# Performance work log

Hardware: AMD Instinct MI355X
Metric: run time of the kernel (lower is better)

The kernel has to match this reference:

```python
import jax, jax.numpy as jnp
import numpy as np

N_HEAD = 16
D_MODEL = 1024
HEAD_DIM = D_MODEL // N_HEAD
B, S = 2, 2048


def setup_inputs() -> dict:
    key = jax.random.key(0)
    ks = jax.random.split(key, 7)
    qry = jax.random.normal(ks[0], (B, S, D_MODEL), dtype=jnp.float32)
    k_in = jax.random.normal(ks[1], (B, S, D_MODEL), dtype=jnp.float32)
    v_in = jax.random.normal(ks[2], (B, S, D_MODEL), dtype=jnp.float32)
    # causal boolean mask (B, S_q, S_k) as asserted in SelfAttention.forward
    attn_mask = jnp.broadcast_to(jnp.tril(jnp.ones((S, S), dtype=bool)), (B, S, S))
    scale = 1.0 / np.sqrt(D_MODEL)
    Wq = jax.random.normal(ks[3], (D_MODEL, D_MODEL), dtype=jnp.float32) * scale
    Wk = jax.random.normal(ks[4], (D_MODEL, D_MODEL), dtype=jnp.float32) * scale
    Wv = jax.random.normal(ks[5], (D_MODEL, D_MODEL), dtype=jnp.float32) * scale
    Wo = jax.random.normal(ks[6], (D_MODEL, D_MODEL), dtype=jnp.float32) * scale
    return {"qry": qry, "key": k_in, "val": v_in, "attn_mask": attn_mask,
            "Wq": Wq, "Wk": Wk, "Wv": Wv, "Wo": Wo}


def reference(qry, key, val, attn_mask, Wq, Wk, Wv, Wo):
    Bq, Sq, _ = qry.shape
    # torch Linear: y = x @ W.T (no bias)
    q = (qry @ Wq.T).reshape(Bq, Sq, N_HEAD, HEAD_DIM).transpose(0, 2, 1, 3)
    k = (key @ Wk.T).reshape(Bq, -1, N_HEAD, HEAD_DIM).transpose(0, 2, 1, 3)
    v = (val @ Wv.T).reshape(Bq, -1, N_HEAD, HEAD_DIM).transpose(0, 2, 1, 3)
    # scores: [B, H, Sq, Sk]
    scores = jnp.einsum('bhqd,bhkd->bhqk', q, k) / jnp.sqrt(jnp.float32(HEAD_DIM * N_HEAD) / N_HEAD)
    # attn_bias: 0 where mask True, -inf where False; broadcast over heads
    bias = jnp.where(attn_mask[:, None, :, :], 0.0, -jnp.inf).astype(scores.dtype)
    attn_weights = jax.nn.softmax(scores + bias, axis=-1)
    attn_feats = jnp.einsum('bhqk,bhkd->bhqd', attn_weights, v)
    attn_feats = attn_feats.transpose(0, 2, 1, 3).reshape(Bq, Sq, D_MODEL)
    output = attn_feats @ Wo.T
    return output, attn_weights
```

## Files before the change

kernel.cpp:

```cpp
#include <hip/hip_runtime.h>
#include <hip/hip_bf16.h>
#include <cstdint>
#include <cstddef>

#define DM 1024
#define NH 16
#define HD 64
#define BB 2
#define SS 2048

typedef __attribute__((ext_vector_type(4))) float f32x4;
typedef __attribute__((ext_vector_type(8))) short bf16x8;

typedef __attribute__((address_space(1))) const void GV;
typedef __attribute__((address_space(3))) void LV;

#define WAITV(N) asm volatile("s_waitcnt vmcnt(" N ")" ::: "memory")
#define SBAR do { __builtin_amdgcn_s_barrier(); asm volatile("" ::: "memory"); } while (0)

__global__ __launch_bounds__(256) void cvt_all(
    const float* s0, const float* s1, const float* s2, const float* s3,
    const float* s4, const float* s5, const float* s6,
    __hip_bfloat16* d0, __hip_bfloat16* d1, __hip_bfloat16* d2, __hip_bfloat16* d3,
    __hip_bfloat16* d4, __hip_bfloat16* d5, __hip_bfloat16* d6) {
    const float* s; __hip_bfloat16* d; int n4;
    switch (blockIdx.y) {
        case 0: s = s0; d = d0; n4 = 1 << 20; break;
        case 1: s = s1; d = d1; n4 = 1 << 20; break;
        case 2: s = s2; d = d2; n4 = 1 << 20; break;
        case 3: s = s3; d = d3; n4 = 1 << 18; break;
        case 4: s = s4; d = d4; n4 = 1 << 18; break;
        case 5: s = s5; d = d5; n4 = 1 << 18; break;
        default: s = s6; d = d6; n4 = 1 << 18; break;
    }
    for (int i = blockIdx.x * 256 + threadIdx.x; i < n4; i += 1024 * 256) {
        float4 v = reinterpret_cast<const float4*>(s)[i];
        ushort4 o;
        o.x = __builtin_bit_cast(unsigned short, __float2bfloat16(v.x));
        o.y = __builtin_bit_cast(unsigned short, __float2bfloat16(v.y));
        o.z = __builtin_bit_cast(unsigned short, __float2bfloat16(v.z));
        o.w = __builtin_bit_cast(unsigned short, __float2bfloat16(v.w));
        reinterpret_cast<ushort4*>(d)[i] = o;
    }
}

template <typename OutT>
__device__ __forceinline__ void gemm_body(const __hip_bfloat16* __restrict__ A,
                                          const __hip_bfloat16* __restrict__ Bw,
                                          OutT* __restrict__ C, int M, int N, int K,
                                          float alpha,
                                          __hip_bfloat16* As, __hip_bfloat16* Bs) {
    const int lane = threadIdx.x & 63;
    const int wv = threadIdx.x >> 6;
    const int wr = wv >> 1, wc = wv & 1;
    const int g = lane >> 4, cq = lane & 15;
    const int tM = blockIdx.y * 128, tN = blockIdx.x * 128;

    f32x4 acc[4][4];
#pragma unroll
    for (int i = 0; i < 4; ++i)
#pragma unroll
        for (int j = 0; j < 4; ++j) acc[i][j] = (f32x4){0.f, 0.f, 0.f, 0.f};

    for (int k0 = 0; k0 < K; k0 += 32) {
        __syncthreads();
#pragma unroll
        for (int r = 0; r < 2; ++r) {
            int chunk = r * 256 + wv * 64 + lane;
            int row = chunk >> 2;
            int kk = (chunk & 3) * 8;
            __builtin_amdgcn_global_load_lds((GV*)(A + (size_t)(tM + row) * K + k0 + kk),
                                             (LV*)(As + (size_t)(r * 256 + wv * 64) * 8), 16, 0, 0);
            __builtin_amdgcn_global_load_lds((GV*)(Bw + (size_t)(tN + row) * K + k0 + kk),
                                             (LV*)(Bs + (size_t)(r * 256 + wv * 64) * 8), 16, 0, 0);
        }
        __syncthreads();

        bf16x8 af[4], bfr[4];
#pragma unroll
        for (int i = 0; i < 4; ++i)
            af[i] = *reinterpret_cast<const bf16x8*>(As + (wr * 64 + i * 16 + cq) * 32 + g * 8);
#pragma unroll
        for (int j = 0; j < 4; ++j)
            bfr[j] = *reinterpret_cast<const bf16x8*>(Bs + (wc * 64 + j * 16 + cq) * 32 + g * 8);
#pragma unroll
        for (int i = 0; i < 4; ++i)
#pragma unroll
            for (int j = 0; j < 4; ++j)
                acc[i][j] = __builtin_amdgcn_mfma_f32_16x16x32_bf16(af[i], bfr[j], acc[i][j], 0, 0, 0);
    }

#pragma unroll
    for (int i = 0; i < 4; ++i)
#pragma unroll
        for (int j = 0; j < 4; ++j)
#pragma unroll
            for (int rr = 0; rr < 4; ++rr) {
                int row = tM + wr * 64 + i * 16 + g * 4 + rr;
                int col = tN + wc * 64 + j * 16 + cq;
                float v = acc[i][j][rr] * alpha;
                if constexpr (__is_same(OutT, float)) {
                    C[(size_t)row * N + col] = v;
                } else {
                    C[(size_t)row * N + col] = __float2bfloat16(v);
                }
            }
}

#define QALPHA 0.1803368801111204f

__global__ __launch_bounds__(256) void gemm_qkv(
    const __hip_bfloat16* qa, const __hip_bfloat16* ka, const __hip_bfloat16* va,
    const __hip_bfloat16* wq, const __hip_bfloat16* wk, const __hip_bfloat16* wv,
    __hip_bfloat16* Qm, __hip_bfloat16* Km, __hip_bfloat16* Vm) {
    __shared__ __hip_bfloat16 As[128 * 32];
    __shared__ __hip_bfloat16 Bs[128 * 32];
    const __hip_bfloat16 *A, *Bw;
    __hip_bfloat16* C;
    float alpha = 1.0f;
    switch (blockIdx.z) {
        case 0: A = qa; Bw = wq; C = Qm; alpha = QALPHA; break;
        case 1: A = ka; Bw = wk; C = Km; break;
        default: A = va; Bw = wv; C = Vm; break;
    }
    gemm_body<__hip_bfloat16>(A, Bw, C, BB * SS, DM, DM, alpha, As, Bs);
}

__global__ __launch_bounds__(256) void gemm_out(const __hip_bfloat16* __restrict__ A,
                                                const __hip_bfloat16* __restrict__ Bw,
                                                float* __restrict__ C) {
    __shared__ __hip_bfloat16 As[128 * 32];
    __shared__ __hip_bfloat16 Bs[128 * 32];
    gemm_body<float>(A, Bw, C, BB * SS, DM, DM, 1.0f, As, Bs);
}

__global__ __launch_bounds__(256) void transpose_v(const __hip_bfloat16* __restrict__ V,
                                                   __hip_bfloat16* __restrict__ VT) {
    const int bh = blockIdx.x;
    const int b = bh >> 4, h = bh & 15;
    const int k0 = blockIdx.y * 64;
    __shared__ __hip_bfloat16 tile[64][68];
    const int r = threadIdx.x >> 4;
    const int c4 = threadIdx.x & 15;
#pragma unroll
    for (int rr = r; rr < 64; rr += 16) {
        ushort4 u = *reinterpret_cast<const ushort4*>(
            V + (size_t)(b * SS + k0 + rr) * DM + h * HD + c4 * 4);
        *reinterpret_cast<ushort4*>(&tile[rr][c4 * 4]) = u;
    }
    __syncthreads();
#pragma unroll
    for (int dd = r; dd < 64; dd += 16) {
        ushort4 o;
        o.x = __builtin_bit_cast(unsigned short, tile[c4 * 4 + 0][dd]);
        o.y = __builtin_bit_cast(unsigned short, tile[c4 * 4 + 1][dd]);
        o.z = __builtin_bit_cast(unsigned short, tile[c4 * 4 + 2][dd]);
        o.w = __builtin_bit_cast(unsigned short, tile[c4 * 4 + 3][dd]);
        *reinterpret_cast<ushort4*>(VT + ((size_t)bh * HD + dd) * SS + k0 + c4 * 4) = o;
    }
}

__global__ __launch_bounds__(256) void attn_fused(const __hip_bfloat16* __restrict__ Q,
                                                  const __hip_bfloat16* __restrict__ Kb,
                                                  const __hip_bfloat16* __restrict__ VT,
                                                  float* __restrict__ Wout,
                                                  __hip_bfloat16* __restrict__ feats) {
    __shared__ __hip_bfloat16 sbuf[4][64 * 64];
    __shared__ __hip_bfloat16 plds[4][16][64];
    const int qt = (SS / 64 - 1) - blockIdx.x;
    const int bh = blockIdx.y;
    const int b = bh >> 4, h = bh & 15;
    const int lane = threadIdx.x & 63;
    const int wv = threadIdx.x >> 6;
    const int g = lane >> 4, cq = lane & 15;
    const int q0w = qt * 64 + wv * 16;
    const size_t rowbase = (size_t)b * SS;
    const int tmaxw = q0w >> 4;

    const __hip_bfloat16* qp = Q + (rowbase + q0w + cq) * DM + h * HD + g * 8;
    const bf16x8 qf0 = *reinterpret_cast<const bf16x8*>(qp);
    const bf16x8 qf1 = *reinterpret_cast<const bf16x8*>(qp + 32);

    auto stageK = [&](int kc, __hip_bfloat16* dst) {
#pragma unroll
        for (int i = 0; i < 2; ++i) {
            int slot = i * 256 + wv * 64 + lane;
            int row = slot >> 3, c16 = slot & 7;
            const __hip_bfloat16* src =
                Kb + (rowbase + kc * 64 + row) * DM + h * HD + ((c16 ^ (row & 7)) << 3);
            __builtin_amdgcn_global_load_lds(
                (GV*)src, (LV*)(dst + (size_t)(i * 256 + wv * 64) * 8), 16, 0, 0);
        }
    };
    auto stageV = [&](int kc, __hip_bfloat16* dst) {
#pragma unroll
        for (int i = 0; i < 2; ++i) {
            int slot = i * 256 + wv * 64 + lane;
            int row = slot >> 3, c16 = slot & 7;
            const __hip_bfloat16* src =
                VT + ((size_t)bh * HD + row) * SS + kc * 64 + ((c16 ^ (row & 7)) << 3);
            __builtin_amdgcn_global_load_lds(
                (GV*)src, (LV*)(dst + (size_t)(i * 256 + wv * 64) * 8), 16, 0, 0);
        }
    };

    const int swx = cq & 7;

    float l_[4] = {0.f, 0.f, 0.f, 0.f};
    stageK(0, sbuf[0]);
    stageK(qt < 1 ? qt : 1, sbuf[1]);
    stageK(qt < 2 ? qt : 2, sbuf[2]);
    WAITV("4");
    SBAR;
    for (int kc = 0; kc <= qt; ++kc) {
        const int nx = kc + 3;
        stageK(nx > qt ? qt : nx, sbuf[nx & 3]);
        const __hip_bfloat16* kbase = sbuf[kc & 3];
#pragma unroll
        for (int hh = 0; hh < 4; ++hh) {
            const int kt = kc * 4 + hh;
            if (kt > tmaxw) break;
            const __hip_bfloat16* kb = kbase + (hh * 16 + cq) * 64;
            bf16x8 kf0 = *reinterpret_cast<const bf16x8*>(kb + ((g ^ swx) << 3));
            bf16x8 kf1 = *reinterpret_cast<const bf16x8*>(kb + (((4 + g) ^ swx) << 3));
            f32x4 sc = (f32x4){0.f, 0.f, 0.f, 0.f};
            sc = __builtin_amdgcn_mfma_f32_16x16x32_bf16(qf0, kf0, sc, 0, 0, 0);
            sc = __builtin_amdgcn_mfma_f32_16x16x32_bf16(qf1, kf1, sc, 0, 0, 0);
            const int kk = kt * 16 + cq;
#pragma unroll
            for (int r = 0; r < 4; ++r) {
                const int qr = q0w + g * 4 + r;
                l_[r] += (kk <= qr) ? __builtin_amdgcn_exp2f(sc[r]) : 0.0f;
            }
        }
        if (kc < qt) {
            WAITV("4");
            SBAR;
        }
    }
    float invl[4];
#pragma unroll
    for (int r = 0; r < 4; ++r) {
        float l = l_[r];
#pragma unroll
        for (int mk = 1; mk < 16; mk <<= 1) l += __shfl_xor(l, mk);
        invl[r] = __builtin_amdgcn_rcpf(l);
    }

    f32x4 oacc[4];
#pragma unroll
    for (int j = 0; j < 4; ++j) oacc[j] = (f32x4){0.f, 0.f, 0.f, 0.f};

    SBAR;
    stageK(0, sbuf[0]);
    stageV(0, sbuf[2]);
    WAITV("0");
    SBAR;
    for (int kc = 0; kc <= qt; ++kc) {
        const int nx = kc + 1;
        const int nc = nx > qt ? qt : nx;
        stageK(nc, sbuf[nx & 1]);
        stageV(nc, sbuf[2 + (nx & 1)]);
        const __hip_bfloat16* kbase = sbuf[kc & 1];
        const __hip_bfloat16* vbase = sbuf[2 + (kc & 1)];

#pragma unroll
        for (int hh = 0; hh < 4; ++hh) {
            const int kt = kc * 4 + hh;
            if (kt <= tmaxw) {
                const __hip_bfloat16* kb = kbase + (hh * 16 + cq) * 64;
                bf16x8 kf0 = *reinterpret_cast<const bf16x8*>(kb + ((g ^ swx) << 3));
                bf16x8 kf1 = *reinterpret_cast<const bf16x8*>(kb + (((4 + g) ^ swx) << 3));
                f32x4 sc = (f32x4){0.f, 0.f, 0.f, 0.f};
                sc = __builtin_amdgcn_mfma_f32_16x16x32_bf16(qf0, kf0, sc, 0, 0, 0);
                sc = __builtin_amdgcn_mfma_f32_16x16x32_bf16(qf1, kf1, sc, 0, 0, 0);
                const int kk = kt * 16 + cq;
#pragma unroll
                for (int r = 0; r < 4; ++r) {
                    const int row = g * 4 + r;
                    const int qr = q0w + row;
                    float w = (kk <= qr) ? __builtin_amdgcn_exp2f(sc[r]) * invl[r] : 0.0f;
                    plds[wv][row][(hh * 16 + cq) ^ (8 * (row & 7))] = __float2bfloat16(w);
                }
            } else {
#pragma unroll
                for (int r = 0; r < 4; ++r) {
                    const int row = g * 4 + r;
                    plds[wv][row][(hh * 16 + cq) ^ (8 * (row & 7))] = __float2bfloat16(0.0f);
                }
            }
        }

        const int sw = 8 * swx;
        bf16x8 wa0 = *reinterpret_cast<const bf16x8*>(&plds[wv][cq][(g * 8) ^ sw]);
        bf16x8 wa1 = *reinterpret_cast<const bf16x8*>(&plds[wv][cq][(32 + g * 8) ^ sw]);
        __builtin_amdgcn_s_setprio(1);
#pragma unroll
        for (int j = 0; j < 4; ++j) {
            const __hip_bfloat16* vb = vbase + (j * 16 + cq) * 64;
            bf16x8 vb0 = *reinterpret_cast<const bf16x8*>(vb + ((g ^ swx) << 3));
            bf16x8 vb1 = *reinterpret_cast<const bf16x8*>(vb + (((4 + g) ^ swx) << 3));
            oacc[j] = __builtin_amdgcn_mfma_f32_16x16x32_bf16(wa0, vb0, oacc[j], 0, 0, 0);
            oacc[j] = __builtin_amdgcn_mfma_f32_16x16x32_bf16(wa1, vb1, oacc[j], 0, 0, 0);
        }
        __builtin_amdgcn_s_setprio(0);

#pragma unroll
        for (int it = 0; it < 4; ++it) {
            const int row = it * 4 + g;
            ushort4 u = *reinterpret_cast<const ushort4*>(
                &plds[wv][row][(cq * 4) ^ (8 * (row & 7))]);
            f32x4 v4;
            v4[0] = __builtin_bit_cast(float, (uint32_t)u.x << 16);
            v4[1] = __builtin_bit_cast(float, (uint32_t)u.y << 16);
            v4[2] = __builtin_bit_cast(float, (uint32_t)u.z << 16);
            v4[3] = __builtin_bit_cast(float, (uint32_t)u.w << 16);
            __builtin_nontemporal_store(
                v4, reinterpret_cast<f32x4*>(
                        Wout + ((size_t)bh * SS + q0w + row) * SS + kc * 64 + cq * 4));
        }

        if (kc < qt) {
            WAITV("4");
            SBAR;
        }
    }

    const int zstart = (qt + 1) * 64;
    const f32x4 z4 = (f32x4){0.f, 0.f, 0.f, 0.f};
    for (int row = 0; row < 16; ++row) {
        float* rp = Wout + ((size_t)bh * SS + q0w + row) * SS;
        for (int c = zstart + lane * 4; c < SS; c += 256)
            __builtin_nontemporal_store(z4, reinterpret_cast<f32x4*>(rp + c));
    }

#pragma unroll
    for (int j = 0; j < 4; ++j)
#pragma unroll
        for (int r = 0; r < 4; ++r)
            feats[(rowbase + q0w + g * 4 + r) * DM + h * HD + j * 16 + cq] =
                __float2bfloat16(oacc[j][r]);
}

extern "C" void kernel_launch(void* const* d_in, const int* in_sizes, int n_in,
                              void* d_out, int out_size, void* d_ws, size_t ws_size,
                              hipStream_t stream) {
    (void)in_sizes; (void)n_in; (void)out_size;
    const float* qry = (const float*)d_in[0];
    const float* key = (const float*)d_in[1];
    const float* val = (const float*)d_in[2];
    const float* Wq = (const float*)d_in[4];
    const float* Wk = (const float*)d_in[5];
    const float* Wv = (const float*)d_in[6];
    const float* Wo = (const float*)d_in[7];

    float* out = (float*)d_out;
    float* w_out = out + (size_t)BB * SS * DM;

    const size_t E = (size_t)BB * SS * DM;
    const size_t W = (size_t)DM * DM;
    if (ws_size < (8 * E + 4 * W) * sizeof(__hip_bfloat16)) return;

    __hip_bfloat16* ws = (__hip_bfloat16*)d_ws;
    __hip_bfloat16* qb    = ws;
    __hip_bfloat16* kb    = ws + E;
    __hip_bfloat16* vb    = ws + 2 * E;
    __hip_bfloat16* wqb   = ws + 3 * E;
    __hip_bfloat16* wkb   = ws + 3 * E + W;
    __hip_bfloat16* wvb   = ws + 3 * E + 2 * W;
    __hip_bfloat16* wob   = ws + 3 * E + 3 * W;
    __hip_bfloat16* Qm    = ws + 3 * E + 4 * W;
    __hip_bfloat16* Km    = ws + 4 * E + 4 * W;
    __hip_bfloat16* Vm    = ws + 5 * E + 4 * W;
    __hip_bfloat16* VTm   = ws + 6 * E + 4 * W;
    __hip_bfloat16* feats = ws + 7 * E + 4 * W;

    cvt_all<<<dim3(1024, 7), 256, 0, stream>>>(qry, key, val, Wq, Wk, Wv, Wo,
                                               qb, kb, vb, wqb, wkb, wvb, wob);

    gemm_qkv<<<dim3(DM / 128, (BB * SS) / 128, 3), 256, 0, stream>>>(
        qb, kb, vb, wqb, wkb, wvb, Qm, Km, Vm);

    transpose_v<<<dim3(BB * NH, SS / 64), 256, 0, stream>>>(Vm, VTm);

    attn_fused<<<dim3(SS / 64, BB * NH), 256, 0, stream>>>(Qm, Km, VTm, w_out, feats);

    gemm_out<<<dim3(DM / 128, (BB * SS) / 128), 256, 0, stream>>>(feats, wob, out);
}
```

Baseline: 262.8 us.

## Process two 64-row query tiles per attention block to reuse staged K/V

Each attention block now handles 128 query rows, with each wave owning two 16-row strips 64 rows apart. Both strips share every staged K and V chunk, which halves the global-to-LDS K/V traffic per query row. The grid shrinks to 16x32 blocks, reducing parallelism and making per-block work less even along the causal diagonal. Register pressure also rises from the doubled Q fragments and accumulators.

Result: slower. 276.4 us (+5.2%).

```diff
diff --git a/kernel.cpp b/kernel.cpp
--- a/kernel.cpp
+++ b/kernel.cpp
@@ -167,19 +167,26 @@
                                                   __hip_bfloat16* __restrict__ feats) {
     __shared__ __hip_bfloat16 sbuf[4][64 * 64];
     __shared__ __hip_bfloat16 plds[4][16][64];
-    const int qt = (SS / 64 - 1) - blockIdx.x;
+    const int qt = (SS / 128 - 1) - blockIdx.x;
     const int bh = blockIdx.y;
     const int b = bh >> 4, h = bh & 15;
     const int lane = threadIdx.x & 63;
     const int wv = threadIdx.x >> 6;
     const int g = lane >> 4, cq = lane & 15;
-    const int q0w = qt * 64 + wv * 16;
+    const int q0a = qt * 128 + wv * 16;
+    const int q0b = q0a + 64;
     const size_t rowbase = (size_t)b * SS;
-    const int tmaxw = q0w >> 4;
-
-    const __hip_bfloat16* qp = Q + (rowbase + q0w + cq) * DM + h * HD + g * 8;
-    const bf16x8 qf0 = *reinterpret_cast<const bf16x8*>(qp);
-    const bf16x8 qf1 = *reinterpret_cast<const bf16x8*>(qp + 32);
+    const int tA = q0a >> 4;
+    const int tB = q0b >> 4;
+    const int kcA = 2 * qt;
+    const int kcmax = 2 * qt + 1;
+
+    const __hip_bfloat16* qpa = Q + (rowbase + q0a + cq) * DM + h * HD + g * 8;
+    const bf16x8 qa0 = *reinterpret_cast<const bf16x8*>(qpa);
+    const bf16x8 qa1 = *reinterpret_cast<const bf16x8*>(qpa + 32);
+    const __hip_bfloat16* qpb = Q + (rowbase + q0b + cq) * DM + h * HD + g * 8;
+    const bf16x8 qb0 = *reinterpret_cast<const bf16x8*>(qpb);
+    const bf16x8 qb1 = *reinterpret_cast<const bf16x8*>(qpb + 32);
 
     auto stageK = [&](int kc, __hip_bfloat16* dst) {
 #pragma unroll
@@ -206,68 +213,81 @@
 
     const int swx = cq & 7;
 
-    float l_[4] = {0.f, 0.f, 0.f, 0.f};
+    float lA[4] = {0.f, 0.f, 0.f, 0.f};
+    float lB[4] = {0.f, 0.f, 0.f, 0.f};
     stageK(0, sbuf[0]);
-    stageK(qt < 1 ? qt : 1, sbuf[1]);
-    stageK(qt < 2 ? qt : 2, sbuf[2]);
+    stageK(kcmax < 1 ? kcmax : 1, sbuf[1]);
+    stageK(kcmax < 2 ? kcmax : 2, sbuf[2]);
     WAITV("4");
     SBAR;
-    for (int kc = 0; kc <= qt; ++kc) {
+    for (int kc = 0; kc <= kcmax; ++kc) {
         const int nx = kc + 3;
-        stageK(nx > qt ? qt : nx, sbuf[nx & 3]);
+        stageK(nx > kcmax ? kcmax : nx, sbuf[nx & 3]);
         const __hip_bfloat16* kbase = sbuf[kc & 3];
+        if (kc <= kcA) {
+#pragma unroll
+            for (int hh = 0; hh < 4; ++hh) {
+                const int kt = kc * 4 + hh;
+                if (kt > tA) break;
+                const __hip_bfloat16* kb = kbase + (hh * 16 + cq) * 64;
+                bf16x8 kf0 = *reinterpret_cast<const bf16x8*>(kb + ((g ^ swx) << 3));
+                bf16x8 kf1 = *reinterpret_cast<const bf16x8*>(kb + (((4 + g) ^ swx) << 3));
+                f32x4 sc = (f32x4){0.f, 0.f, 0.f, 0.f};
+                sc = __builtin_amdgcn_mfma_f32_16x16x32_bf16(qa0, kf0, sc, 0, 0, 0);
+                sc = __builtin_amdgcn_mfma_f32_16x16x32_bf16(qa1, kf1, sc, 0, 0, 0);
+                const int kk = kt * 16 + cq;
+#pragma unroll
+                for (int r = 0; r < 4; ++r)
+                    lA[r] += (kk <= q0a + g * 4 + r) ? __builtin_amdgcn_exp2f(sc[r]) : 0.0f;
+            }
+        }
 #pragma unroll
         for (int hh = 0; hh < 4; ++hh) {
             const int kt = kc * 4 + hh;
-            if (kt > tmaxw) break;
+            if (kt > tB) break;
             const __hip_bfloat16* kb = kbase + (hh * 16 + cq) * 64;
             bf16x8 kf0 = *reinterpret_cast<const bf16x8*>(kb + ((g ^ swx) << 3));
             bf16x8 kf1 = *reinterpret_cast<const bf16x8*>(kb + (((4 + g) ^ swx) << 3));
             f32x4 sc = (f32x4){0.f, 0.f, 0.f, 0.f};
-            sc = __builtin_amdgcn_mfma_f32_16x16x32_bf16(qf0, kf0, sc, 0, 0, 0);
-            sc = __builtin_amdgcn_mfma_f32_16x16x32_bf16(qf1, kf1, sc, 0, 0, 0);
+            sc = __builtin_amdgcn_mfma_f32_16x16x32_bf16(qb0, kf0, sc, 0, 0, 0);
+            sc = __builtin_amdgcn_mfma_f32_16x16x32_bf16(qb1, kf1, sc, 0, 0, 0);
             const int kk = kt * 16 + cq;
 #pragma unroll
-            for (int r = 0; r < 4; ++r) {
-                const int qr = q0w + g * 4 + r;
-                l_[r] += (kk <= qr) ? __builtin_amdgcn_exp2f(sc[r]) : 0.0f;
-            }
-        }
-        if (kc < qt) {
+            for (int r = 0; r < 4; ++r)
+                lB[r] += (kk <= q0b + g * 4 + r) ? __builtin_amdgcn_exp2f(sc[r]) : 0.0f;
+        }
+        if (kc < kcmax) {
             WAITV("4");
             SBAR;
         }
     }
-    float invl[4];
+    float invlA[4], invlB[4];
 #pragma unroll
     for (int r = 0; r < 4; ++r) {
-        float l = l_[r];
-#pragma unroll
-        for (int mk = 1; mk < 16; mk <<= 1) l += __shfl_xor(l, mk);
-        invl[r] = __builtin_amdgcn_rcpf(l);
-    }
-
-    f32x4 oacc[4];
-#pragma unroll
-    for (int j = 0; j < 4; ++j) oacc[j] = (f32x4){0.f, 0.f, 0.f, 0.f};
-
-    SBAR;
-    stageK(0, sbuf[0]);
-    stageV(0, sbuf[2]);
-    WAITV("0");
-    SBAR;
-    for (int kc = 0; kc <= qt; ++kc) {
-        const int nx = kc + 1;
-        const int nc = nx > qt ? qt : nx;
-        stageK(nc, sbuf[nx & 1]);
-        stageV(nc, sbuf[2 + (nx & 1)]);
-        const __hip_bfloat16* kbase = sbuf[kc & 1];
-        const __hip_bfloat16* vbase = sbuf[2 + (kc & 1)];
-
+        float la = lA[r], lb = lB[r];
+#pragma unroll
+        for (int mk = 1; mk < 16; mk <<= 1) {
+            la += __shfl_xor(la, mk);
+            lb += __shfl_xor(lb, mk);
+        }
+        invlA[r] = __builtin_amdgcn_rcpf(la);
+        invlB[r] = __builtin_amdgcn_rcpf(lb);
+    }
+
+    f32x4 oaccA[4], oaccB[4];
+#pragma unroll
+    for (int j = 0; j < 4; ++j) {
+        oaccA[j] = (f32x4){0.f, 0.f, 0.f, 0.f};
+        oaccB[j] = (f32x4){0.f, 0.f, 0.f, 0.f};
+    }
+
+    auto doSub = [&](const bf16x8& qf0, const bf16x8& qf1, int tmax_, int q0_,
+                     const float* invl_, f32x4 (&oacc_)[4],
+                     const __hip_bfloat16* kbase, const __hip_bfloat16* vbase, int kc) {
 #pragma unroll
         for (int hh = 0; hh < 4; ++hh) {
             const int kt = kc * 4 + hh;
-            if (kt <= tmaxw) {
+            if (kt <= tmax_) {
                 const __hip_bfloat16* kb = kbase + (hh * 16 + cq) * 64;
                 bf16x8 kf0 = *reinterpret_cast<const bf16x8*>(kb + ((g ^ swx) << 3));
                 bf16x8 kf1 = *reinterpret_cast<const bf16x8*>(kb + (((4 + g) ^ swx) << 3));
@@ -278,8 +298,7 @@
 #pragma unroll
                 for (int r = 0; r < 4; ++r) {
                     const int row = g * 4 + r;
-                    const int qr = q0w + row;
-                    float w = (kk <= qr) ? __builtin_amdgcn_exp2f(sc[r]) * invl[r] : 0.0f;
+                    float w = (kk <= q0_ + row) ? __builtin_amdgcn_exp2f(sc[r]) * invl_[r] : 0.0f;
                     plds[wv][row][(hh * 16 + cq) ^ (8 * (row & 7))] = __float2bfloat16(w);
                 }
             } else {
@@ -297,11 +316,11 @@
         __builtin_amdgcn_s_setprio(1);
 #pragma unroll
         for (int j = 0; j < 4; ++j) {
-            const __hip_bfloat16* vb = vbase + (j * 16 + cq) * 64;
-            bf16x8 vb0 = *reinterpret_cast<const bf16x8*>(vb + ((g ^ swx) << 3));
-            bf16x8 vb1 = *reinterpret_cast<const bf16x8*>(vb + (((4 + g) ^ swx) << 3));
-            oacc[j] = __builtin_amdgcn_mfma_f32_16x16x32_bf16(wa0, vb0, oacc[j], 0, 0, 0);
-            oacc[j] = __builtin_amdgcn_mfma_f32_16x16x32_bf16(wa1, vb1, oacc[j], 0, 0, 0);
+            const __hip_bfloat16* vp = vbase + (j * 16 + cq) * 64;
+            bf16x8 v0 = *reinterpret_cast<const bf16x8*>(vp + ((g ^ swx) << 3));
+            bf16x8 v1 = *reinterpret_cast<const bf16x8*>(vp + (((4 + g) ^ swx) << 3));
+            oacc_[j] = __builtin_amdgcn_mfma_f32_16x16x32_bf16(wa0, v0, oacc_[j], 0, 0, 0);
+            oacc_[j] = __builtin_amdgcn_mfma_f32_16x16x32_bf16(wa1, v1, oacc_[j], 0, 0, 0);
         }
         __builtin_amdgcn_s_setprio(0);
 
@@ -317,29 +336,55 @@
             v4[3] = __builtin_bit_cast(float, (uint32_t)u.w << 16);
             __builtin_nontemporal_store(
                 v4, reinterpret_cast<f32x4*>(
-                        Wout + ((size_t)bh * SS + q0w + row) * SS + kc * 64 + cq * 4));
-        }
-
-        if (kc < qt) {
+                        Wout + ((size_t)bh * SS + q0_ + row) * SS + kc * 64 + cq * 4));
+        }
+    };
+
+    SBAR;
+    stageK(0, sbuf[0]);
+    stageV(0, sbuf[2]);
+    WAITV("0");
+    SBAR;
+    for (int kc = 0; kc <= kcmax; ++kc) {
+        const int nx = kc + 1;
+        const int nc = nx > kcmax ? kcmax : nx;
+        stageK(nc, sbuf[nx & 1]);
+        stageV(nc, sbuf[2 + (nx & 1)]);
+        const __hip_bfloat16* kbase = sbuf[kc & 1];
+        const __hip_bfloat16* vbase = sbuf[2 + (kc & 1)];
+
+        if (kc <= kcA) doSub(qa0, qa1, tA, q0a, invlA, oaccA, kbase, vbase, kc);
+        doSub(qb0, qb1, tB, q0b, invlB, oaccB, kbase, vbase, kc);
+
+        if (kc < kcmax) {
             WAITV("4");
             SBAR;
         }
     }
 
-    const int zstart = (qt + 1) * 64;
     const f32x4 z4 = (f32x4){0.f, 0.f, 0.f, 0.f};
+    const int zA = (kcA + 1) * 64;
     for (int row = 0; row < 16; ++row) {
-        float* rp = Wout + ((size_t)bh * SS + q0w + row) * SS;
-        for (int c = zstart + lane * 4; c < SS; c += 256)
+        float* rp = Wout + ((size_t)bh * SS + q0a + row) * SS;
+        for (int c = zA + lane * 4; c < SS; c += 256)
             __builtin_nontemporal_store(z4, reinterpret_cast<f32x4*>(rp + c));
     }
+    const int zB = (kcmax + 1) * 64;
+    for (int row = 0; row < 16; ++row) {
+        float* rp = Wout + ((size_t)bh * SS + q0b + row) * SS;
+        for (int c = zB + lane * 4; c < SS; c += 256)
+            __builtin_nontemporal_store(z4, reinterpret_cast<f32x4*>(rp + c));
+    }
 
 #pragma unroll
     for (int j = 0; j < 4; ++j)
 #pragma unroll
-        for (int r = 0; r < 4; ++r)
-            feats[(rowbase + q0w + g * 4 + r) * DM + h * HD + j * 16 + cq] =
-                __float2bfloat16(oacc[j][r]);
+        for (int r = 0; r < 4; ++r) {
+            feats[(rowbase + q0a + g * 4 + r) * DM + h * HD + j * 16 + cq] =
+                __float2bfloat16(oaccA[j][r]);
+            feats[(rowbase + q0b + g * 4 + r) * DM + h * HD + j * 16 + cq] =
+                __float2bfloat16(oaccB[j][r]);
+        }
 }
 
 extern "C" void kernel_launch(void* const* d_in, const int* in_sizes, int n_in,
@@ -383,7 +428,7 @@
 
     transpose_v<<<dim3(BB * NH, SS / 64), 256, 0, stream>>>(Vm, VTm);
 
-    attn_fused<<<dim3(SS / 64, BB * NH), 256, 0, stream>>>(Qm, Km, VTm, w_out, feats);
+    attn_fused<<<dim3(SS / 128, BB * NH), 256, 0, stream>>>(Qm, Km, VTm, w_out, feats);
 
     gemm_out<<<dim3(DM / 128, (BB * SS) / 128), 256, 0, stream>>>(feats, wob, out);
 }
```
